# Performance work log

Hardware: AMD Instinct MI355X
Metric: run time of the kernel (lower is better)

## Reference

```python
import jax, jax.numpy as jnp
import numpy as np

E = 384      # dim_embd
H = 6        # n_heads
D = E // H   # head dim = 64
T_MAX = 256  # block_size
EPS = 1e-5


def setup_inputs() -> dict:
    key = jax.random.key(0)
    ks = jax.random.split(key, 12)
    B, T = 128, 256
    s_in = (1.0 / E) ** 0.5
    s_ff = (1.0 / (4 * E)) ** 0.5
    return {
        "x": jax.random.normal(ks[0], (B, T, E), jnp.float32),
        # per-head projections stacked to match torch concat order: [E, H*D]
        "wq": jax.random.normal(ks[1], (E, E), jnp.float32) * s_in,
        "wk": jax.random.normal(ks[2], (E, E), jnp.float32) * s_in,
        "wv": jax.random.normal(ks[3], (E, E), jnp.float32) * s_in,
        "w_proj": jax.random.normal(ks[4], (E, E), jnp.float32) * s_in,
        "b_proj": jnp.zeros((E,), jnp.float32),
        "w1": jax.random.normal(ks[5], (E, 4 * E), jnp.float32) * s_in,
        "b1": jnp.zeros((4 * E,), jnp.float32),
        "w2": jax.random.normal(ks[6], (4 * E, E), jnp.float32) * s_ff,
        "b2": jnp.zeros((E,), jnp.float32),
        "g1": jnp.ones((E,), jnp.float32),
        "beta1": jnp.zeros((E,), jnp.float32),
        "g2": jnp.ones((E,), jnp.float32),
        "beta2": jnp.zeros((E,), jnp.float32),
    }


def _layernorm(x, g, b):
    mu = jnp.mean(x, axis=-1, keepdims=True)
    var = jnp.mean(jnp.square(x - mu), axis=-1, keepdims=True)
    return (x - mu) * jax.lax.rsqrt(var + EPS) * g + b


def _attention(x, wq, wk, wv, w_proj, b_proj):
    B, T, C = x.shape
    # batched per-head projections: [B,T,H,D]
    q = (x @ wq).reshape(B, T, H, D)
    k = (x @ wk).reshape(B, T, H, D)
    v = (x @ wv).reshape(B, T, H, D)
    # NOTE: original scales by C**-0.5 with C = full embed dim (384)
    scale = C ** (-0.5)
    scores = jnp.einsum("bthd,bshd->bhts", q, k) * scale
    mask = jnp.tril(jnp.ones((T, T), bool))
    scores = jnp.where(mask, scores, -jnp.inf)
    wei = jax.nn.softmax(scores, axis=-1)  # dropout = identity (eval)
    out = jnp.einsum("bhts,bshd->bthd", wei, v).reshape(B, T, C)
    return out @ w_proj + b_proj


def reference(x, wq, wk, wv, w_proj, b_proj, w1, b1, w2, b2, g1, beta1, g2, beta2):
    x = x + _attention(_layernorm(x, g1, beta1), wq, wk, wv, w_proj, b_proj)
    h = _layernorm(x, g2, beta2)
    h = jax.nn.relu(h @ w1 + b1) @ w2 + b2  # dropout = identity (eval)
    return x + h
```

## Files before the change

### kernel.cpp

```cpp
#include <hip/hip_runtime.h>
#include <hip/hip_bf16.h>

typedef __attribute__((ext_vector_type(8))) short bf16x8;
typedef __attribute__((ext_vector_type(4))) float f32x4;

#define MFMA_BF16(a, b, c) __builtin_amdgcn_mfma_f32_16x16x32_bf16((a), (b), (c), 0, 0, 0)

#define E_DIM 384
#define T_SEQ 256
#define B_BATCH 128
#define H_HEADS 6
#define D_HEAD 64
#define NROWS (B_BATCH * T_SEQ)
#define FF_DIM (4 * E_DIM)
#define QKV_LD 1152

__device__ __forceinline__ void load_lds16(const __hip_bfloat16* g, __hip_bfloat16* l) {
    __builtin_amdgcn_global_load_lds(
        (const __attribute__((address_space(1))) void*)g,
        (__attribute__((address_space(3))) void*)l, 16, 0, 0);
}

__global__ void tcast_all_kernel(const float* __restrict__ wq, const float* __restrict__ wk,
                                 const float* __restrict__ wv, const float* __restrict__ wp,
                                 const float* __restrict__ w1, const float* __restrict__ w2,
                                 __hip_bfloat16* __restrict__ wqkvT, __hip_bfloat16* __restrict__ wpT,
                                 __hip_bfloat16* __restrict__ w1T, __hip_bfloat16* __restrict__ w2T) {
    const int WE = E_DIM * E_DIM;
    const int FE = E_DIM * FF_DIM;
    int idx = blockIdx.x * 256 + threadIdx.x;
    if (idx < 3 * WE) {
        int seg = idx / WE, j = idx - seg * WE;
        const float* W = seg == 0 ? wq : (seg == 1 ? wk : wv);
        int k = j / E_DIM, n = j - k * E_DIM;
        wqkvT[(size_t)seg * WE + (size_t)n * E_DIM + k] = __float2bfloat16(W[j]);
    } else if (idx < 4 * WE) {
        int j = idx - 3 * WE;
        int k = j / E_DIM, n = j - k * E_DIM;
        wpT[(size_t)n * E_DIM + k] = __float2bfloat16(wp[j]);
    } else if (idx < 4 * WE + FE) {
        int j = idx - 4 * WE;
        int k = j / FF_DIM, n = j - k * FF_DIM;
        w1T[(size_t)n * E_DIM + k] = __float2bfloat16(w1[j]);
    } else {
        int j = idx - 4 * WE - FE;
        int k = j / E_DIM, n = j - k * E_DIM;
        w2T[(size_t)n * FF_DIM + k] = __float2bfloat16(w2[j]);
    }
}

__global__ __launch_bounds__(256) void ln_kernel(const float* __restrict__ x,
                                                 const float* __restrict__ g,
                                                 const float* __restrict__ bta,
                                                 __hip_bfloat16* __restrict__ out) {
    int row = blockIdx.x * 4 + (threadIdx.x >> 6);
    int lane = threadIdx.x & 63;
    const float* xr = x + (size_t)row * E_DIM;
    float vals[6];
    float s = 0.f;
#pragma unroll
    for (int i = 0; i < 6; i++) {
        vals[i] = xr[lane + i * 64];
        s += vals[i];
    }
#pragma unroll
    for (int off = 1; off < 64; off <<= 1) s += __shfl_xor(s, off, 64);
    float mu = s * (1.f / E_DIM);
    float vv = 0.f;
#pragma unroll
    for (int i = 0; i < 6; i++) {
        float d = vals[i] - mu;
        vv += d * d;
    }
#pragma unroll
    for (int off = 1; off < 64; off <<= 1) vv += __shfl_xor(vv, off, 64);
    float rstd = rsqrtf(vv * (1.f / E_DIM) + 1e-5f);
#pragma unroll
    for (int i = 0; i < 6; i++) {
        int c = lane + i * 64;
        out[(size_t)row * E_DIM + c] =
            __float2bfloat16((vals[i] - mu) * rstd * g[c] + bta[c]);
    }
}

template <int EPI>
__global__ __launch_bounds__(512, 4) void gemm_k32_kernel(
    const __hip_bfloat16* __restrict__ A, const __hip_bfloat16* __restrict__ BT,
    const float* __restrict__ bias, const float* __restrict__ resid,
    __hip_bfloat16* __restrict__ outb, float* __restrict__ outf,
    int M, int N, int K) {
    __shared__ __hip_bfloat16 lds[3 * 12288];
    const int t = threadIdx.x;
    const int w = t >> 6, lane = t & 63;
    const int l16 = lane & 15, lhi = lane >> 4;
    const int wm = w >> 1, wn = w & 1;

    const int nwg = gridDim.x;
    const int bid = blockIdx.x;
    const int cpx = nwg >> 3;
    const int swz = (bid & 7) * cpx + (bid >> 3);
    const int nb = N >> 7;
    const int m0 = (swz / nb) * 256;
    const int n0 = (swz % nb) * 128;

    const int srow = t >> 2;
    const int sslot = t & 3;
    const int scol = ((sslot ^ (srow & 3) ^ ((srow >> 2) & 3)) << 3);
    const __hip_bfloat16* pa0 = A + (size_t)(m0 + srow) * K + scol;
    const __hip_bfloat16* pa1 = A + (size_t)(m0 + 128 + srow) * K + scol;
    const __hip_bfloat16* pb0 = BT + (size_t)(n0 + srow) * K + scol;
    const int dstA = t * 8;

    int aoff[4], boff[4];
#pragma unroll
    for (int mr = 0; mr < 4; mr++) {
        int R = wm * 64 + mr * 16 + l16;
        int slot = lhi ^ (R & 3) ^ ((R >> 2) & 3);
        aoff[mr] = R * 32 + slot * 8;
    }
#pragma unroll
    for (int nr = 0; nr < 4; nr++) {
        int R = wn * 64 + nr * 16 + l16;
        int slot = lhi ^ (R & 3) ^ ((R >> 2) & 3);
        boff[nr] = 8192 + R * 32 + slot * 8;
    }

    f32x4 acc[4][4] = {};
    const int nk = K >> 5;

#define STAGE(sbuf)                                                           \
    {                                                                         \
        __hip_bfloat16* sbase = &lds[(sbuf) * 12288];                         \
        load_lds16(pa0, sbase + dstA);                                        \
        load_lds16(pa1, sbase + 4096 + dstA);                                 \
        load_lds16(pb0, sbase + 8192 + dstA);                                 \
        pa0 += 32;                                                            \
        pa1 += 32;                                                            \
        pb0 += 32;                                                            \
    }

    STAGE(0);
    STAGE(1);
    int rb = 0, sb = 2;

    for (int kt = 0; kt < nk; kt++) {
        if (kt + 1 < nk) {
            asm volatile("s_waitcnt vmcnt(3)" ::: "memory");
        } else {
            asm volatile("s_waitcnt vmcnt(0)" ::: "memory");
        }
        __builtin_amdgcn_s_barrier();
        __builtin_amdgcn_sched_barrier(0);
        if (kt + 2 < nk) STAGE(sb);
        const __hip_bfloat16* base = &lds[rb * 12288];
        bf16x8 af[4], bg[4];
#pragma unroll
        for (int mr = 0; mr < 4; mr++)
            af[mr] = *reinterpret_cast<const bf16x8*>(base + aoff[mr]);
#pragma unroll
        for (int nr = 0; nr < 4; nr++)
            bg[nr] = *reinterpret_cast<const bf16x8*>(base + boff[nr]);
        __builtin_amdgcn_s_setprio(1);
#pragma unroll
        for (int mr = 0; mr < 4; mr++)
#pragma unroll
            for (int nr = 0; nr < 4; nr++)
                acc[mr][nr] = MFMA_BF16(af[mr], bg[nr], acc[mr][nr]);
        __builtin_amdgcn_s_setprio(0);
        rb = rb == 2 ? 0 : rb + 1;
        sb = sb == 2 ? 0 : sb + 1;
    }
#undef STAGE

#pragma unroll
    for (int mr = 0; mr < 4; mr++) {
#pragma unroll
        for (int nr = 0; nr < 4; nr++) {
            int col = n0 + wn * 64 + nr * 16 + l16;
#pragma unroll
            for (int r = 0; r < 4; r++) {
                int row = m0 + wm * 64 + mr * 16 + lhi * 4 + r;
                size_t off = (size_t)row * N + col;
                float v = acc[mr][nr][r];
                if (EPI == 0) {
                    outb[off] = __float2bfloat16(v);
                } else if (EPI == 1) {
                    outf[off] = v + bias[col] + resid[off];
                } else {
                    v += bias[col];
                    outb[off] = __float2bfloat16(v > 0.f ? v : 0.f);
                }
            }
        }
    }
}

__global__ __launch_bounds__(512, 1) void attn_kernel(
    const __hip_bfloat16* __restrict__ qkv, __hip_bfloat16* __restrict__ o) {
    __shared__ __hip_bfloat16 Ks[T_SEQ][72];
    __shared__ __hip_bfloat16 VTs[D_HEAD][264];
    __shared__ __hip_bfloat16 Ps[8][32][72];

    const int bh = blockIdx.x;
    const int b = bh / H_HEADS, h = bh - b * H_HEADS;
    const int t = threadIdx.x;
    const int w = t >> 6, lane = t & 63;
    const int l16 = lane & 15, lhi = lane >> 4;
    const size_t rbase = (size_t)b * T_SEQ;
    const int qoff = h * D_HEAD, koff = E_DIM + h * D_HEAD, voff = 2 * E_DIM + h * D_HEAD;
    const float qscale = 0.051031036307982884f * 1.4426950408889634f;

    bf16x8 qf[2][2];
#pragma unroll
    for (int mr = 0; mr < 2; mr++)
#pragma unroll
        for (int kk = 0; kk < 2; kk++)
            qf[mr][kk] = *reinterpret_cast<const bf16x8*>(
                qkv + (rbase + w * 32 + mr * 16 + l16) * QKV_LD + qoff + kk * 32 + lhi * 8);

#pragma unroll
    for (int i = 0; i < 4; i++) {
        int idx = i * 512 + t;
        int r = idx >> 3, c = (idx & 7) * 8;
        *reinterpret_cast<uint4*>(&Ks[r][c]) =
            *reinterpret_cast<const uint4*>(qkv + (rbase + r) * QKV_LD + koff + c);
    }
#pragma unroll
    for (int i = 0; i < 4; i++) {
        int idx = i * 512 + t;
        int r = idx >> 3, d0 = (idx & 7) * 8;
        uint4 val = *reinterpret_cast<const uint4*>(qkv + (rbase + r) * QKV_LD + voff + d0);
        const __hip_bfloat16* p8 = reinterpret_cast<const __hip_bfloat16*>(&val);
#pragma unroll
        for (int j = 0; j < 8; j++) VTs[d0 + j][r] = p8[j];
    }
    __syncthreads();

    float mstate[2][4], lstate[2][4];
    f32x4 oacc[2][4] = {};
#pragma unroll
    for (int mr = 0; mr < 2; mr++)
#pragma unroll
        for (int r = 0; r < 4; r++) {
            mstate[mr][r] = -1e30f;
            lstate[mr][r] = 0.f;
        }

    const int njt = (w >> 1) + 1;
    for (int jt = 0; jt < njt; jt++) {
        const bool diag = (jt == (w >> 1));
        f32x4 s[2][4] = {};
#pragma unroll
        for (int kk = 0; kk < 2; kk++) {
            bf16x8 kf[4];
#pragma unroll
            for (int nr = 0; nr < 4; nr++)
                kf[nr] = *reinterpret_cast<const bf16x8*>(
                    &Ks[jt * 64 + nr * 16 + l16][kk * 32 + lhi * 8]);
#pragma unroll
            for (int mr = 0; mr < 2; mr++)
#pragma unroll
                for (int nr = 0; nr < 4; nr++)
                    s[mr][nr] = MFMA_BF16(qf[mr][kk], kf[nr], s[mr][nr]);
        }
#pragma unroll
        for (int mr = 0; mr < 2; mr++) {
#pragma unroll
            for (int r = 0; r < 4; r++) {
                int qrow = w * 32 + mr * 16 + lhi * 4 + r;
                float pv[4];
                float mx = -1e30f;
                if (diag) {
#pragma unroll
                    for (int nr = 0; nr < 4; nr++) {
                        int kcol = jt * 64 + nr * 16 + l16;
                        float val = s[mr][nr][r] * qscale;
                        if (kcol > qrow) val = -1e30f;
                        pv[nr] = val;
                        mx = fmaxf(mx, val);
                    }
                } else {
#pragma unroll
                    for (int nr = 0; nr < 4; nr++) {
                        float val = s[mr][nr][r] * qscale;
                        pv[nr] = val;
                        mx = fmaxf(mx, val);
                    }
                }
#pragma unroll
                for (int off = 1; off < 16; off <<= 1)
                    mx = fmaxf(mx, __shfl_xor(mx, off, 64));
                float mold = mstate[mr][r];
                float mnew = fmaxf(mold, mx);
                float corr = exp2f(mold - mnew);
                float psum = 0.f;
#pragma unroll
                for (int nr = 0; nr < 4; nr++) {
                    float p = exp2f(pv[nr] - mnew);
                    pv[nr] = p;
                    psum += p;
                }
#pragma unroll
                for (int off = 1; off < 16; off <<= 1)
                    psum += __shfl_xor(psum, off, 64);
                lstate[mr][r] = lstate[mr][r] * corr + psum;
                mstate[mr][r] = mnew;
#pragma unroll
                for (int dr = 0; dr < 4; dr++) oacc[mr][dr][r] *= corr;
#pragma unroll
                for (int nr = 0; nr < 4; nr++)
                    Ps[w][mr * 16 + lhi * 4 + r][nr * 16 + l16] = __float2bfloat16(pv[nr]);
            }
        }
#pragma unroll
        for (int kk = 0; kk < 2; kk++) {
            bf16x8 pa[2], vbf[4];
#pragma unroll
            for (int mr = 0; mr < 2; mr++)
                pa[mr] = *reinterpret_cast<const bf16x8*>(
                    &Ps[w][mr * 16 + l16][kk * 32 + lhi * 8]);
#pragma unroll
            for (int dr = 0; dr < 4; dr++)
                vbf[dr] = *reinterpret_cast<const bf16x8*>(
                    &VTs[dr * 16 + l16][jt * 64 + kk * 32 + lhi * 8]);
#pragma unroll
            for (int mr = 0; mr < 2; mr++)
#pragma unroll
                for (int dr = 0; dr < 4; dr++)
                    oacc[mr][dr] = MFMA_BF16(pa[mr], vbf[dr], oacc[mr][dr]);
        }
    }

#pragma unroll
    for (int mr = 0; mr < 2; mr++) {
#pragma unroll
        for (int r = 0; r < 4; r++) {
            float rl = 1.f / lstate[mr][r];
            int row = w * 32 + mr * 16 + lhi * 4 + r;
#pragma unroll
            for (int dr = 0; dr < 4; dr++)
                o[(rbase + row) * E_DIM + h * D_HEAD + dr * 16 + l16] =
                    __float2bfloat16(oacc[mr][dr][r] * rl);
        }
    }
}

extern "C" void kernel_launch(void* const* d_in, const int* in_sizes, int n_in,
                              void* d_out, int out_size, void* d_ws, size_t ws_size,
                              hipStream_t stream) {
    const float* x      = (const float*)d_in[0];
    const float* wq     = (const float*)d_in[1];
    const float* wk     = (const float*)d_in[2];
    const float* wv     = (const float*)d_in[3];
    const float* w_proj = (const float*)d_in[4];
    const float* b_proj = (const float*)d_in[5];
    const float* w1     = (const float*)d_in[6];
    const float* b1     = (const float*)d_in[7];
    const float* w2     = (const float*)d_in[8];
    const float* b2     = (const float*)d_in[9];
    const float* g1     = (const float*)d_in[10];
    const float* bt1    = (const float*)d_in[11];
    const float* g2     = (const float*)d_in[12];
    const float* bt2    = (const float*)d_in[13];
    float* out = (float*)d_out;

    char* ws = (char*)d_ws;
    size_t off = 0;
    auto alloc = [&](size_t bytes) {
        void* p = ws + off;
        off += (bytes + 255) & ~(size_t)255;
        return p;
    };
    const size_t wElems = E_DIM * E_DIM;
    const size_t fElems = E_DIM * FF_DIM;
    const size_t actElems = (size_t)NROWS * E_DIM;
    __hip_bfloat16* wqkvT = (__hip_bfloat16*)alloc(3 * wElems * 2);
    __hip_bfloat16* wpT   = (__hip_bfloat16*)alloc(wElems * 2);
    __hip_bfloat16* w1T   = (__hip_bfloat16*)alloc(fElems * 2);
    __hip_bfloat16* w2T   = (__hip_bfloat16*)alloc(fElems * 2);
    __hip_bfloat16* lnb   = (__hip_bfloat16*)alloc(actElems * 2);
    __hip_bfloat16* qkv   = (__hip_bfloat16*)alloc(3 * actElems * 2);
    __hip_bfloat16* ab    = (__hip_bfloat16*)alloc(actElems * 2);
    __hip_bfloat16* h1    = qkv;
    float* x2 = out;

    tcast_all_kernel<<<6912, 256, 0, stream>>>(wq, wk, wv, w_proj, w1, w2,
                                               wqkvT, wpT, w1T, w2T);

    ln_kernel<<<NROWS / 4, 256, 0, stream>>>(x, g1, bt1, lnb);

    gemm_k32_kernel<0><<<(NROWS / 256) * (QKV_LD / 128), 512, 0, stream>>>(
        lnb, wqkvT, nullptr, nullptr, qkv, nullptr, NROWS, QKV_LD, E_DIM);

    attn_kernel<<<B_BATCH * H_HEADS, 512, 0, stream>>>(qkv, ab);

    gemm_k32_kernel<1><<<(NROWS / 256) * (E_DIM / 128), 512, 0, stream>>>(
        ab, wpT, b_proj, x, nullptr, x2, NROWS, E_DIM, E_DIM);

    ln_kernel<<<NROWS / 4, 256, 0, stream>>>(x2, g2, bt2, lnb);

    gemm_k32_kernel<2><<<(NROWS / 256) * (FF_DIM / 128), 512, 0, stream>>>(
        lnb, w1T, b1, nullptr, h1, nullptr, NROWS, FF_DIM, E_DIM);

    gemm_k32_kernel<1><<<(NROWS / 256) * (E_DIM / 128), 512, 0, stream>>>(
        h1, w2T, b2, x2, nullptr, out, NROWS, E_DIM, FF_DIM);
}
```

Measured before the change: 256.0 us.

## Vectorize GEMM epilogues, store residual in bf16, use smaller tiles for N=384 GEMMs

Swaps the MFMA operand order so each lane holds four consecutive columns, which lets epilogue stores be vectorized (packed bf16x4 or float4) in place of scalar stores. The intermediate residual x2 is now kept in bf16 instead of fp32, which cuts traffic for the second LayerNorm and the final residual read. The two N=384 GEMMs use a 4-wave 128-row tile variant to get more workgroups. The risk is lower precision in the residual stream, since x2 is rounded to bf16 before being added to the output.

```diff
diff --git a/kernel.cpp b/kernel.cpp
--- a/kernel.cpp
+++ b/kernel.cpp
@@ -19,6 +19,15 @@
     __builtin_amdgcn_global_load_lds(
         (const __attribute__((address_space(1))) void*)g,
         (__attribute__((address_space(3))) void*)l, 16, 0, 0);
+}
+
+__device__ __forceinline__ uint2 pack4bf(f32x4 v) {
+    union { __hip_bfloat16 h[4]; uint2 u; } cv;
+    cv.h[0] = __float2bfloat16(v[0]);
+    cv.h[1] = __float2bfloat16(v[1]);
+    cv.h[2] = __float2bfloat16(v[2]);
+    cv.h[3] = __float2bfloat16(v[3]);
+    return cv.u;
 }
 
 __global__ void tcast_all_kernel(const float* __restrict__ wq, const float* __restrict__ wk,
@@ -49,18 +58,22 @@
     }
 }
 
-__global__ __launch_bounds__(256) void ln_kernel(const float* __restrict__ x,
+__device__ __forceinline__ float to_f(float x) { return x; }
+__device__ __forceinline__ float to_f(__hip_bfloat16 x) { return __bfloat162float(x); }
+
+template <typename TI>
+__global__ __launch_bounds__(256) void ln_kernel(const TI* __restrict__ x,
                                                  const float* __restrict__ g,
                                                  const float* __restrict__ bta,
                                                  __hip_bfloat16* __restrict__ out) {
     int row = blockIdx.x * 4 + (threadIdx.x >> 6);
     int lane = threadIdx.x & 63;
-    const float* xr = x + (size_t)row * E_DIM;
+    const TI* xr = x + (size_t)row * E_DIM;
     float vals[6];
     float s = 0.f;
 #pragma unroll
     for (int i = 0; i < 6; i++) {
-        vals[i] = xr[lane + i * 64];
+        vals[i] = to_f(xr[lane + i * 64]);
         s += vals[i];
     }
 #pragma unroll
@@ -83,13 +96,15 @@
     }
 }
 
-template <int EPI>
-__global__ __launch_bounds__(512, 4) void gemm_k32_kernel(
+template <int EPI, int NW>
+__global__ __launch_bounds__(NW * 64, NW == 8 ? 4 : 3) void gemm_kernel(
     const __hip_bfloat16* __restrict__ A, const __hip_bfloat16* __restrict__ BT,
-    const float* __restrict__ bias, const float* __restrict__ resid,
-    __hip_bfloat16* __restrict__ outb, float* __restrict__ outf,
-    int M, int N, int K) {
-    __shared__ __hip_bfloat16 lds[3 * 12288];
+    const float* __restrict__ bias, const void* __restrict__ resid,
+    void* __restrict__ outp, int M, int N, int K) {
+    constexpr int BM = NW * 32;
+    constexpr int T = NW * 64;
+    constexpr int BUF = (BM + 128) * 32;
+    __shared__ __hip_bfloat16 lds[3 * BUF];
     const int t = threadIdx.x;
     const int w = t >> 6, lane = t & 63;
     const int l16 = lane & 15, lhi = lane >> 4;
@@ -100,15 +115,16 @@
     const int cpx = nwg >> 3;
     const int swz = (bid & 7) * cpx + (bid >> 3);
     const int nb = N >> 7;
-    const int m0 = (swz / nb) * 256;
+    const int m0 = (swz / nb) * BM;
     const int n0 = (swz % nb) * 128;
 
     const int srow = t >> 2;
     const int sslot = t & 3;
     const int scol = ((sslot ^ (srow & 3) ^ ((srow >> 2) & 3)) << 3);
     const __hip_bfloat16* pa0 = A + (size_t)(m0 + srow) * K + scol;
-    const __hip_bfloat16* pa1 = A + (size_t)(m0 + 128 + srow) * K + scol;
+    const __hip_bfloat16* pa1 = pa0 + (size_t)(BM / 2) * K;
     const __hip_bfloat16* pb0 = BT + (size_t)(n0 + srow) * K + scol;
+    const __hip_bfloat16* pb1 = pb0 + (size_t)64 * K;
     const int dstA = t * 8;
 
     int aoff[4], boff[4];
@@ -122,37 +138,37 @@
     for (int nr = 0; nr < 4; nr++) {
         int R = wn * 64 + nr * 16 + l16;
         int slot = lhi ^ (R & 3) ^ ((R >> 2) & 3);
-        boff[nr] = 8192 + R * 32 + slot * 8;
+        boff[nr] = BM * 32 + R * 32 + slot * 8;
     }
 
     f32x4 acc[4][4] = {};
     const int nk = K >> 5;
 
-#define STAGE(sbuf)                                                           \
-    {                                                                         \
-        __hip_bfloat16* sbase = &lds[(sbuf) * 12288];                         \
-        load_lds16(pa0, sbase + dstA);                                        \
-        load_lds16(pa1, sbase + 4096 + dstA);                                 \
-        load_lds16(pb0, sbase + 8192 + dstA);                                 \
-        pa0 += 32;                                                            \
-        pa1 += 32;                                                            \
-        pb0 += 32;                                                            \
-    }
+    auto STAGE = [&](int sbuf) {
+        __hip_bfloat16* sb_ = &lds[sbuf * BUF];
+        load_lds16(pa0, sb_ + dstA);
+        load_lds16(pa1, sb_ + T * 8 + dstA);
+        load_lds16(pb0, sb_ + BM * 32 + dstA);
+        if constexpr (NW == 4) load_lds16(pb1, sb_ + BM * 32 + 2048 + dstA);
+        pa0 += 32; pa1 += 32; pb0 += 32;
+        if constexpr (NW == 4) pb1 += 32;
+    };
 
     STAGE(0);
     STAGE(1);
-    int rb = 0, sb = 2;
+    int rb = 0, sbx = 2;
 
     for (int kt = 0; kt < nk; kt++) {
         if (kt + 1 < nk) {
-            asm volatile("s_waitcnt vmcnt(3)" ::: "memory");
+            if constexpr (NW == 8) asm volatile("s_waitcnt vmcnt(3)" ::: "memory");
+            else                   asm volatile("s_waitcnt vmcnt(4)" ::: "memory");
         } else {
             asm volatile("s_waitcnt vmcnt(0)" ::: "memory");
         }
         __builtin_amdgcn_s_barrier();
         __builtin_amdgcn_sched_barrier(0);
-        if (kt + 2 < nk) STAGE(sb);
-        const __hip_bfloat16* base = &lds[rb * 12288];
+        if (kt + 2 < nk) STAGE(sbx);
+        const __hip_bfloat16* base = &lds[rb * BUF];
         bf16x8 af[4], bg[4];
 #pragma unroll
         for (int mr = 0; mr < 4; mr++)
@@ -165,31 +181,41 @@
         for (int mr = 0; mr < 4; mr++)
 #pragma unroll
             for (int nr = 0; nr < 4; nr++)
-                acc[mr][nr] = MFMA_BF16(af[mr], bg[nr], acc[mr][nr]);
+                acc[mr][nr] = MFMA_BF16(bg[nr], af[mr], acc[mr][nr]);
         __builtin_amdgcn_s_setprio(0);
         rb = rb == 2 ? 0 : rb + 1;
-        sb = sb == 2 ? 0 : sb + 1;
-    }
-#undef STAGE
+        sbx = sbx == 2 ? 0 : sbx + 1;
+    }
 
 #pragma unroll
     for (int mr = 0; mr < 4; mr++) {
+        const int grow = m0 + wm * 64 + mr * 16 + l16;
 #pragma unroll
         for (int nr = 0; nr < 4; nr++) {
-            int col = n0 + wn * 64 + nr * 16 + l16;
-#pragma unroll
-            for (int r = 0; r < 4; r++) {
-                int row = m0 + wm * 64 + mr * 16 + lhi * 4 + r;
-                size_t off = (size_t)row * N + col;
-                float v = acc[mr][nr][r];
-                if (EPI == 0) {
-                    outb[off] = __float2bfloat16(v);
-                } else if (EPI == 1) {
-                    outf[off] = v + bias[col] + resid[off];
-                } else {
-                    v += bias[col];
-                    outb[off] = __float2bfloat16(v > 0.f ? v : 0.f);
-                }
+            const int gcol = n0 + wn * 64 + nr * 16 + lhi * 4;
+            const size_t off = (size_t)grow * N + gcol;
+            f32x4 v = acc[mr][nr];
+            if (EPI != 0) {
+                const float4 bv = *reinterpret_cast<const float4*>(&bias[gcol]);
+                v[0] += bv.x; v[1] += bv.y; v[2] += bv.z; v[3] += bv.w;
+            }
+            if (EPI == 2) {
+#pragma unroll
+                for (int j = 0; j < 4; j++) v[j] = v[j] > 0.f ? v[j] : 0.f;
+            }
+            if (EPI == 3) {
+                const float4 rv = *reinterpret_cast<const float4*>((const float*)resid + off);
+                v[0] += rv.x; v[1] += rv.y; v[2] += rv.z; v[3] += rv.w;
+            }
+            if (EPI == 4) {
+                union { uint2 u; __hip_bfloat16 h[4]; } rv;
+                rv.u = *reinterpret_cast<const uint2*>((const __hip_bfloat16*)resid + off);
+#pragma unroll
+                for (int j = 0; j < 4; j++) v[j] += __bfloat162float(rv.h[j]);
+                float4 st = {v[0], v[1], v[2], v[3]};
+                *reinterpret_cast<float4*>((float*)outp + off) = st;
+            } else {
+                *reinterpret_cast<uint2*>((__hip_bfloat16*)outp + off) = pack4bf(v);
             }
         }
     }
@@ -379,29 +405,29 @@
     __hip_bfloat16* w1T   = (__hip_bfloat16*)alloc(fElems * 2);
     __hip_bfloat16* w2T   = (__hip_bfloat16*)alloc(fElems * 2);
     __hip_bfloat16* lnb   = (__hip_bfloat16*)alloc(actElems * 2);
+    __hip_bfloat16* x2b   = (__hip_bfloat16*)alloc(actElems * 2);
     __hip_bfloat16* qkv   = (__hip_bfloat16*)alloc(3 * actElems * 2);
     __hip_bfloat16* ab    = (__hip_bfloat16*)alloc(actElems * 2);
     __hip_bfloat16* h1    = qkv;
-    float* x2 = out;
 
     tcast_all_kernel<<<6912, 256, 0, stream>>>(wq, wk, wv, w_proj, w1, w2,
                                                wqkvT, wpT, w1T, w2T);
 
-    ln_kernel<<<NROWS / 4, 256, 0, stream>>>(x, g1, bt1, lnb);
-
-    gemm_k32_kernel<0><<<(NROWS / 256) * (QKV_LD / 128), 512, 0, stream>>>(
-        lnb, wqkvT, nullptr, nullptr, qkv, nullptr, NROWS, QKV_LD, E_DIM);
+    ln_kernel<float><<<NROWS / 4, 256, 0, stream>>>(x, g1, bt1, lnb);
+
+    gemm_kernel<0, 8><<<(NROWS / 256) * (QKV_LD / 128), 512, 0, stream>>>(
+        lnb, wqkvT, nullptr, nullptr, qkv, NROWS, QKV_LD, E_DIM);
 
     attn_kernel<<<B_BATCH * H_HEADS, 512, 0, stream>>>(qkv, ab);
 
-    gemm_k32_kernel<1><<<(NROWS / 256) * (E_DIM / 128), 512, 0, stream>>>(
-        ab, wpT, b_proj, x, nullptr, x2, NROWS, E_DIM, E_DIM);
-
-    ln_kernel<<<NROWS / 4, 256, 0, stream>>>(x2, g2, bt2, lnb);
-
-    gemm_k32_kernel<2><<<(NROWS / 256) * (FF_DIM / 128), 512, 0, stream>>>(
-        lnb, w1T, b1, nullptr, h1, nullptr, NROWS, FF_DIM, E_DIM);
-
-    gemm_k32_kernel<1><<<(NROWS / 256) * (E_DIM / 128), 512, 0, stream>>>(
-        h1, w2T, b2, x2, nullptr, out, NROWS, E_DIM, FF_DIM);
-}
+    gemm_kernel<3, 4><<<(NROWS / 128) * (E_DIM / 128), 256, 0, stream>>>(
+        ab, wpT, b_proj, x, x2b, NROWS, E_DIM, E_DIM);
+
+    ln_kernel<__hip_bfloat16><<<NROWS / 4, 256, 0, stream>>>(x2b, g2, bt2, lnb);
+
+    gemm_kernel<2, 8><<<(NROWS / 256) * (FF_DIM / 128), 512, 0, stream>>>(
+        lnb, w1T, b1, nullptr, h1, NROWS, FF_DIM, E_DIM);
+
+    gemm_kernel<4, 4><<<(NROWS / 128) * (E_DIM / 128), 256, 0, stream>>>(
+        h1, w2T, b2, x2b, out, NROWS, E_DIM, FF_DIM);
+}
```

Result: slower. 281.7 us (+10.0%).
